# Kernel tuning notes

Measured on AMD Instinct MI355X. Metric: run time of the kernel, lower is better.

Reference implementation:

```python
import jax, jax.numpy as jnp
import numpy as np

NUM_USERS = 100000
NUM_BOOKS = 50000
HIDDEN = 128
USER_FEAT = 256
BOOK_FEAT = 256
E_PER_REL = 500000
NUM_LAYERS = 2


def setup_inputs() -> dict:
    key = jax.random.key(0)
    ks = jax.random.split(key, 10)
    user_x = jax.random.normal(ks[0], (NUM_USERS, USER_FEAT), dtype=jnp.float32)
    book_x = jax.random.normal(ks[1], (NUM_BOOKS, BOOK_FEAT), dtype=jnp.float32)
    user_W = jax.random.normal(ks[2], (HIDDEN, USER_FEAT), dtype=jnp.float32) * 0.05
    user_b = jax.random.normal(ks[3], (HIDDEN,), dtype=jnp.float32) * 0.05
    book_W = jax.random.normal(ks[4], (HIDDEN, BOOK_FEAT), dtype=jnp.float32) * 0.05
    book_b = jax.random.normal(ks[5], (HIDDEN,), dtype=jnp.float32) * 0.05
    # edge_index[0] = user indices, edge_index[1] = book indices
    rates_edge = jnp.stack([
        jax.random.randint(ks[6], (E_PER_REL,), 0, NUM_USERS),
        jax.random.randint(ks[7], (E_PER_REL,), 0, NUM_BOOKS)])
    implicit_edge = jnp.stack([
        jax.random.randint(ks[8], (E_PER_REL,), 0, NUM_USERS),
        jax.random.randint(ks[9], (E_PER_REL,), 0, NUM_BOOKS)])
    return {"user_x": user_x, "book_x": book_x, "user_W": user_W,
            "user_b": user_b, "book_W": book_W, "book_b": book_b,
            "rates_edge": rates_edge, "implicit_edge": implicit_edge}


def _lightgcn(user_x, book_x, user_W, user_b, book_W, book_b, rates_edge, implicit_edge):
    num_users = user_x.shape[0]
    num_nodes = num_users + book_x.shape[0]
    # input projections
    cu = user_x @ user_W.T + user_b  # [U, H]
    cb = book_x @ book_W.T + book_b  # [B, H]
    user_embeds = [cu]
    book_embeds = [cb]
    # build full directed edge list exactly as in the torch source
    all_edges = jnp.concatenate([rates_edge, implicit_edge], axis=1)  # [2, E]
    book_to_user = jnp.stack([all_edges[1] + num_users, all_edges[0]])
    full_edge = jnp.concatenate([all_edges, book_to_user], axis=1)  # [2, 2E]
    row, col = full_edge[0], full_edge[1]
    # symmetric degree normalization (edges fixed across layers)
    deg = jax.ops.segment_sum(jnp.ones(col.shape, dtype=cu.dtype), col,
                              num_segments=num_nodes)
    deg_inv_sqrt = jnp.where(deg > 0, jax.lax.rsqrt(jnp.maximum(deg, 1.0) * 0 + jnp.where(deg > 0, deg, 1.0)), 0.0)
    deg_inv_sqrt = jnp.where(deg > 0, jax.lax.rsqrt(jnp.where(deg > 0, deg, 1.0)), 0.0)
    norm = deg_inv_sqrt[row] * deg_inv_sqrt[col]  # [2E]
    for _ in range(NUM_LAYERS):
        x = jnp.concatenate([cu, cb], axis=0)  # [U+B, H]
        msg = x[row] * norm[:, None]           # gather + scale, [2E, H]
        out = jax.ops.segment_sum(msg, col, num_segments=num_nodes)  # scatter-add
        cu = out[:num_users]
        cb = out[num_users:]
        user_embeds.append(cu)
        book_embeds.append(cb)
    final_user = jnp.mean(jnp.stack(user_embeds), axis=0)
    final_book = jnp.mean(jnp.stack(book_embeds), axis=0)
    return final_user, final_book


def reference(user_x, book_x, user_W, user_b, book_W, book_b, rates_edge, implicit_edge):
    return _lightgcn(user_x, book_x, user_W, user_b, book_W, book_b,
                     rates_edge, implicit_edge)
```

## Files before the change

### kernel.cpp

```cpp
#include <hip/hip_runtime.h>

#define NUSERS 100000
#define NBOOKS 50000
#define HID 128
#define FEAT 256
#define EPR 500000
#define NEDGE (2 * EPR)

#define UBLK ((NUSERS + 127) / 128)
#define BBLK ((NBOOKS + 127) / 128)
#define GEMM_BLOCKS (UBLK + BBLK)
#define HIST_BLOCKS ((NEDGE + 1023) / 1024)

typedef __attribute__((ext_vector_type(8))) short bf16x8;
typedef __attribute__((ext_vector_type(4))) float f32x4;

__device__ __forceinline__ unsigned short f2bf(float f) {
  union { float f; unsigned u; } v; v.f = f;
  unsigned r = v.u + 0x7FFFu + ((v.u >> 16) & 1u);
  return (unsigned short)(r >> 16);
}
__device__ __forceinline__ float bf2f(unsigned short h) {
  union { unsigned u; float f; } v; v.u = ((unsigned)h) << 16;
  return v.f;
}

__global__ void cast_w(const float* __restrict__ w0, const float* __restrict__ w1,
                       unsigned short* __restrict__ o0, unsigned short* __restrict__ o1)
{
  int i = blockIdx.x * 256 + threadIdx.x;
  if (i < HID * FEAT) { o0[i] = f2bf(w0[i]); o1[i] = f2bf(w1[i]); }
}

__device__ __forceinline__ void decode_edge(const int* __restrict__ rates,
                                            const int* __restrict__ impl,
                                            int i, int& u, int& bk)
{
  if (i < EPR) { u = rates[i]; bk = rates[EPR + i]; }
  else { int j = i - EPR; u = impl[j]; bk = impl[EPR + j]; }
}

__global__ __launch_bounds__(256) void gemm_hist(
    const float* __restrict__ Xu, const float* __restrict__ Xb,
    const unsigned short* __restrict__ Wu, const unsigned short* __restrict__ Wb,
    const float* __restrict__ bu, const float* __restrict__ bb,
    unsigned short* __restrict__ cu0b, float* __restrict__ outb,
    float* __restrict__ outu,
    const int* __restrict__ rates, const int* __restrict__ impl,
    int* __restrict__ degu, int* __restrict__ cntb,
    unsigned int* __restrict__ relpos)
{
  __shared__ float Abuf[2][128 * 32];
  const int bid = blockIdx.x;
  const int tid = threadIdx.x;

  if (bid >= GEMM_BLOCKS) {
    const int hb = bid - GEMM_BLOCKS;
#pragma unroll
    for (int q = 0; q < 4; ++q) {
      int i = hb * 1024 + q * 256 + tid;
      if (i < NEDGE) {
        int u, bk;
        decode_edge(rates, impl, i, u, bk);
        relpos[i] = (unsigned int)atomicAdd(&cntb[bk], 1);
        atomicAdd(&degu[u], 1);
      }
    }
    return;
  }

  const bool isU = bid < UBLK;
  const float* __restrict__ X = isU ? Xu : Xb;
  const unsigned short* __restrict__ W = isU ? Wu : Wb;
  const float* __restrict__ bias = isU ? bu : bb;
  const int M  = isU ? NUSERS : NBOOKS;
  const int bm = (isU ? bid : bid - UBLK) * 128;

  const int lane = tid & 63;
  const int wv   = tid >> 6;
  const int l15  = lane & 15, l4 = lane >> 4;
  const int row0 = wv * 32;

  auto stage = [&](int bf, int ks) {
    const int k0 = ks * 32;
#pragma unroll
    for (int q = 0; q < 4; ++q) {
      int o = q * 256 + tid;
      int r = o >> 3;
      int s = (o & 7) ^ (r & 7);
      int gr = bm + r; if (gr > M - 1) gr = M - 1;
      const float* src = &X[(size_t)gr * FEAT + k0 + s * 4];
      float* dst = &Abuf[bf][(size_t)(q * 256 + wv * 64) * 4];
      __builtin_amdgcn_global_load_lds(src, dst, 16, 0, 0);
    }
  };

  f32x4 acc[2][8];
#pragma unroll
  for (int mi = 0; mi < 2; ++mi)
#pragma unroll
    for (int ni = 0; ni < 8; ++ni) acc[mi][ni] = (f32x4)0.f;

  stage(0, 0);

#pragma unroll
  for (int ks = 0; ks < 8; ++ks) {
    if (ks < 7) stage((ks + 1) & 1, ks + 1);
    __syncthreads();
    const float* Ab = Abuf[ks & 1];

    bf16x8 bfr[8];
#pragma unroll
    for (int ni = 0; ni < 8; ++ni) {
      int col = ni * 16 + l15;
      bfr[ni] = *reinterpret_cast<const bf16x8*>(&W[(size_t)col * FEAT + ks * 32 + l4 * 8]);
    }

    bf16x8 a[2];
#pragma unroll
    for (int mi = 0; mi < 2; ++mi) {
      int rt = row0 + mi * 16 + l15;
      int m7 = rt & 7;
      int s0 = l4 * 2;
      float4 x0 = *reinterpret_cast<const float4*>(&Ab[rt * 32 + ((s0)     ^ m7) * 4]);
      float4 x1 = *reinterpret_cast<const float4*>(&Ab[rt * 32 + ((s0 + 1) ^ m7) * 4]);
      bf16x8 av;
      av[0] = (short)f2bf(x0.x); av[1] = (short)f2bf(x0.y);
      av[2] = (short)f2bf(x0.z); av[3] = (short)f2bf(x0.w);
      av[4] = (short)f2bf(x1.x); av[5] = (short)f2bf(x1.y);
      av[6] = (short)f2bf(x1.z); av[7] = (short)f2bf(x1.w);
      a[mi] = av;
    }

#pragma unroll
    for (int ni = 0; ni < 8; ++ni) {
      acc[0][ni] = __builtin_amdgcn_mfma_f32_16x16x32_bf16(a[0], bfr[ni], acc[0][ni], 0, 0, 0);
      acc[1][ni] = __builtin_amdgcn_mfma_f32_16x16x32_bf16(a[1], bfr[ni], acc[1][ni], 0, 0, 0);
    }
    __syncthreads();
  }

#pragma unroll
  for (int ni = 0; ni < 8; ++ni) {
    int col = ni * 16 + l15;
    float bj = bias[col];
#pragma unroll
    for (int mi = 0; mi < 2; ++mi) {
#pragma unroll
      for (int j = 0; j < 4; ++j) {
        int rr = bm + row0 + mi * 16 + l4 * 4 + j;
        if (rr < M) {
          float vv = acc[mi][ni][j] + bj;
          if (isU) {
            cu0b[(size_t)rr * HID + col] = f2bf(vv);
            if (rr >= NBOOKS) outu[(size_t)rr * HID + col] = vv * (1.0f / 3.0f);
          } else {
            outb[(size_t)rr * HID + col] = vv * (1.0f / 3.0f);
          }
        }
      }
    }
  }
}

__global__ void dis_kernel(const int* __restrict__ degu, const int* __restrict__ cntb,
                           float* __restrict__ dis)
{
  int i = blockIdx.x * blockDim.x + threadIdx.x;
  if (i < NUSERS) {
    int d = degu[i] + (i < NBOOKS ? cntb[i] : 0);
    dis[i] = (d > 0) ? rsqrtf((float)d) : 0.f;
  }
}

__global__ void fill_scatter(const int* __restrict__ rates, const int* __restrict__ impl,
                             const int* __restrict__ offs,
                             const unsigned int* __restrict__ relpos,
                             int* __restrict__ brow)
{
  int i = blockIdx.x * blockDim.x + threadIdx.x;
  if (i >= NEDGE) return;
  int u, bk;
  decode_edge(rates, impl, i, u, bk);
  brow[offs[bk] + (int)relpos[i]] = u;
}

__global__ __launch_bounds__(1024) void scan_blocks(const int* __restrict__ counts,
                                                    int* __restrict__ offs,
                                                    int* __restrict__ bsum, int N)
{
  __shared__ int buf[1024];
  int t = threadIdx.x;
  int i = blockIdx.x * 1024 + t;
  int v = (i < N) ? counts[i] : 0;
  buf[t] = v;
  __syncthreads();
  for (int off = 1; off < 1024; off <<= 1) {
    int x = (t >= off) ? buf[t - off] : 0;
    __syncthreads();
    buf[t] += x;
    __syncthreads();
  }
  int incl = buf[t];
  if (i < N) offs[i] = incl - v;
  if (t == 1023) bsum[blockIdx.x] = incl;
}

__global__ void scan_totals(const int* __restrict__ bsum, int* __restrict__ bpre,
                            int* __restrict__ offs, int nb, int N)
{
  if (threadIdx.x == 0 && blockIdx.x == 0) {
    int run = 0;
    for (int b = 0; b < nb; ++b) { bpre[b] = run; run += bsum[b]; }
    offs[N] = run;
  }
}

__global__ void add_prefix(int* __restrict__ offs, const int* __restrict__ bpre, int N)
{
  int i = blockIdx.x * blockDim.x + threadIdx.x;
  if (i < N) offs[i] += bpre[i >> 10];
}

__global__ __launch_bounds__(256) void pull1(const unsigned short* __restrict__ srcb,
    const int* __restrict__ offs, const int* __restrict__ brow,
    const float* __restrict__ dis, unsigned short* __restrict__ dstb)
{
  int c = (blockIdx.x << 2) + (threadIdx.x >> 6);
  if (c >= NBOOKS) return;
  const int lane = threadIdx.x & 63;
  const int g = lane >> 4, l = lane & 15;
  const int s = offs[c], e = offs[c + 1];

  float acc[8];
#pragma unroll
  for (int j = 0; j < 8; ++j) acc[j] = 0.f;

  int i = s + g;
  for (; i + 4 < e; i += 8) {
    int rr0 = brow[i], rr1 = brow[i + 4];
    float w0 = dis[rr0], w1 = dis[rr1];
    bf16x8 v0 = *reinterpret_cast<const bf16x8*>(&srcb[(size_t)rr0 * HID + l * 8]);
    bf16x8 v1 = *reinterpret_cast<const bf16x8*>(&srcb[(size_t)rr1 * HID + l * 8]);
#pragma unroll
    for (int j = 0; j < 8; ++j) acc[j] += w0 * bf2f((unsigned short)v0[j]);
#pragma unroll
    for (int j = 0; j < 8; ++j) acc[j] += w1 * bf2f((unsigned short)v1[j]);
  }
  if (i < e) {
    int rr = brow[i];
    float w = dis[rr];
    bf16x8 v = *reinterpret_cast<const bf16x8*>(&srcb[(size_t)rr * HID + l * 8]);
#pragma unroll
    for (int j = 0; j < 8; ++j) acc[j] += w * bf2f((unsigned short)v[j]);
  }

#pragma unroll
  for (int j = 0; j < 8; ++j) {
    acc[j] += __shfl_xor(acc[j], 16, 64);
    acc[j] += __shfl_xor(acc[j], 32, 64);
  }
  if (g == 0) {
    float db = dis[c];
    bf16x8 o;
#pragma unroll
    for (int j = 0; j < 8; ++j) o[j] = (short)f2bf(db * acc[j]);
    *reinterpret_cast<bf16x8*>(&dstb[(size_t)c * HID + l * 8]) = o;
  }
}

__global__ __launch_bounds__(256) void pull2_final(const unsigned short* __restrict__ h1b,
    const int* __restrict__ offs, const int* __restrict__ brow,
    const float* __restrict__ dis, const unsigned short* __restrict__ cu0b,
    float* __restrict__ outu)
{
  int c = (blockIdx.x << 2) + (threadIdx.x >> 6);
  if (c >= NBOOKS) return;
  const int lane = threadIdx.x & 63;
  const int g = lane >> 4, l = lane & 15;
  const int s = offs[c], e = offs[c + 1];

  float acc[8];
#pragma unroll
  for (int j = 0; j < 8; ++j) acc[j] = 0.f;

  int i = s + g;
  for (; i + 4 < e; i += 8) {
    int rr0 = brow[i], rr1 = brow[i + 4];
    int rc0 = rr0 < NBOOKS ? rr0 : 0;
    int rc1 = rr1 < NBOOKS ? rr1 : 0;
    float w0 = rr0 < NBOOKS ? dis[rr0] : 0.f;
    float w1 = rr1 < NBOOKS ? dis[rr1] : 0.f;
    bf16x8 v0 = *reinterpret_cast<const bf16x8*>(&h1b[(size_t)rc0 * HID + l * 8]);
    bf16x8 v1 = *reinterpret_cast<const bf16x8*>(&h1b[(size_t)rc1 * HID + l * 8]);
#pragma unroll
    for (int j = 0; j < 8; ++j) acc[j] += w0 * bf2f((unsigned short)v0[j]);
#pragma unroll
    for (int j = 0; j < 8; ++j) acc[j] += w1 * bf2f((unsigned short)v1[j]);
  }
  if (i < e) {
    int rr = brow[i];
    int rc = rr < NBOOKS ? rr : 0;
    float w = rr < NBOOKS ? dis[rr] : 0.f;
    bf16x8 v = *reinterpret_cast<const bf16x8*>(&h1b[(size_t)rc * HID + l * 8]);
#pragma unroll
    for (int j = 0; j < 8; ++j) acc[j] += w * bf2f((unsigned short)v[j]);
  }

#pragma unroll
  for (int j = 0; j < 8; ++j) {
    acc[j] += __shfl_xor(acc[j], 16, 64);
    acc[j] += __shfl_xor(acc[j], 32, 64);
  }
  if (g == 0) {
    float db = dis[c];
    size_t idx = (size_t)c * HID + l * 8;
    bf16x8 c0 = *reinterpret_cast<const bf16x8*>(&cu0b[idx]);
    bf16x8 h1 = *reinterpret_cast<const bf16x8*>(&h1b[idx]);
    float r[8];
#pragma unroll
    for (int j = 0; j < 8; ++j)
      r[j] = (bf2f((unsigned short)c0[j]) + bf2f((unsigned short)h1[j]) + db * acc[j]) * (1.0f / 3.0f);
    *reinterpret_cast<float4*>(&outu[idx])     = make_float4(r[0], r[1], r[2], r[3]);
    *reinterpret_cast<float4*>(&outu[idx + 4]) = make_float4(r[4], r[5], r[6], r[7]);
  }
}

extern "C" void kernel_launch(void* const* d_in, const int* in_sizes, int n_in,
                              void* d_out, int out_size, void* d_ws, size_t ws_size,
                              hipStream_t stream)
{
  const float* user_x = (const float*)d_in[0];
  const float* book_x = (const float*)d_in[1];
  const float* user_W = (const float*)d_in[2];
  const float* user_b = (const float*)d_in[3];
  const float* book_W = (const float*)d_in[4];
  const float* book_b = (const float*)d_in[5];
  const int*   rates  = (const int*)d_in[6];
  const int*   impl   = (const int*)d_in[7];

  float* out      = (float*)d_out;
  float* out_user = out;
  float* out_book = out + (size_t)NUSERS * HID;

  char* p = (char*)d_ws;
  auto carve = [&](size_t bytes) -> void* {
    void* r = (void*)p;
    p += (bytes + 255) & ~(size_t)255;
    return r;
  };
  unsigned short* cu0b   = (unsigned short*)carve((size_t)NUSERS * HID * 2);
  unsigned short* h1b    = (unsigned short*)carve((size_t)NBOOKS * HID * 2);
  unsigned short* wub    = (unsigned short*)carve((size_t)HID * FEAT * 2);
  unsigned short* wbb    = (unsigned short*)carve((size_t)HID * FEAT * 2);
  int*          degu   = (int*)carve((size_t)NUSERS * 4);
  int*          cntb   = (int*)carve((size_t)NBOOKS * 4);
  float*        dis    = (float*)carve((size_t)NUSERS * 4);
  int*          offs   = (int*)carve((size_t)(NBOOKS + 2) * 4);
  int*          bsum   = (int*)carve(256 * 4);
  int*          bpre   = (int*)carve(256 * 4);
  unsigned int* relpos = (unsigned int*)carve((size_t)NEDGE * 4);
  int*          brow   = (int*)carve((size_t)NEDGE * 4);

  hipMemsetAsync(degu, 0, (size_t)NUSERS * 4, stream);
  hipMemsetAsync(cntb, 0, (size_t)NBOOKS * 4, stream);

  cast_w<<<(HID * FEAT + 255) / 256, 256, 0, stream>>>(user_W, book_W, wub, wbb);

  gemm_hist<<<GEMM_BLOCKS + HIST_BLOCKS, 256, 0, stream>>>(
      user_x, book_x, wub, wbb, user_b, book_b,
      cu0b, out_book, out_user, rates, impl, degu, cntb, relpos);

  dis_kernel<<<(NUSERS + 255) / 256, 256, 0, stream>>>(degu, cntb, dis);

  const int nb = (NBOOKS + 1023) / 1024;
  scan_blocks<<<nb, 1024, 0, stream>>>(cntb, offs, bsum, NBOOKS);
  scan_totals<<<1, 64, 0, stream>>>(bsum, bpre, offs, nb, NBOOKS);
  add_prefix<<<(NBOOKS + 255) / 256, 256, 0, stream>>>(offs, bpre, NBOOKS);
  fill_scatter<<<(NEDGE + 255) / 256, 256, 0, stream>>>(rates, impl, offs, relpos, brow);

  pull1<<<(NBOOKS + 3) / 4, 256, 0, stream>>>(cu0b, offs, brow, dis, h1b);
  pull2_final<<<(NBOOKS + 3) / 4, 256, 0, stream>>>(h1b, offs, brow, dis, cu0b, out_user);
}
```

Baseline: 258.9 us.

## Interleave histogram and GEMM blocks, stage bf16 A tile, fuse dis into fill

The combined GEMM/histogram kernel now interleaves histogram blocks with GEMM blocks so atomic-heavy edge counting runs concurrently with the projection instead of trailing it. The GEMM A tile is loaded through registers, converted to bf16 once, and stored in a swizzled 128x128 LDS buffer in two halves, replacing the double-buffered fp32 async-to-LDS pipeline and the per-iteration conversion. The degree inverse-sqrt kernel is merged into the edge fill-scatter launch to remove one launch. The change gives up async load overlap within the GEMM in exchange for fewer conversions and fewer barriers.

```diff
diff --git a/kernel.cpp b/kernel.cpp
--- a/kernel.cpp
+++ b/kernel.cpp
@@ -11,6 +11,8 @@
 #define BBLK ((NBOOKS + 127) / 128)
 #define GEMM_BLOCKS (UBLK + BBLK)
 #define HIST_BLOCKS ((NEDGE + 1023) / 1024)
+#define FILL_B ((NEDGE + 255) / 256)
+#define DIS_B ((NUSERS + 255) / 256)
 
 typedef __attribute__((ext_vector_type(8))) short bf16x8;
 typedef __attribute__((ext_vector_type(4))) float f32x4;
@@ -50,94 +52,100 @@
     int* __restrict__ degu, int* __restrict__ cntb,
     unsigned int* __restrict__ relpos)
 {
-  __shared__ float Abuf[2][128 * 32];
+  __shared__ unsigned short Asb[128 * 128];
   const int bid = blockIdx.x;
   const int tid = threadIdx.x;
 
-  if (bid >= GEMM_BLOCKS) {
-    const int hb = bid - GEMM_BLOCKS;
-#pragma unroll
-    for (int q = 0; q < 4; ++q) {
-      int i = hb * 1024 + q * 256 + tid;
-      if (i < NEDGE) {
-        int u, bk;
-        decode_edge(rates, impl, i, u, bk);
-        relpos[i] = (unsigned int)atomicAdd(&cntb[bk], 1);
-        atomicAdd(&degu[u], 1);
-      }
-    }
-    return;
-  }
-
-  const bool isU = bid < UBLK;
+  int gid;
+  if (bid < 2 * HIST_BLOCKS) {
+    if (bid & 1) {
+      const int hb = bid >> 1;
+#pragma unroll
+      for (int q = 0; q < 4; ++q) {
+        int i = hb * 1024 + q * 256 + tid;
+        if (i < NEDGE) {
+          int u, bk;
+          decode_edge(rates, impl, i, u, bk);
+          relpos[i] = (unsigned int)atomicAdd(&cntb[bk], 1);
+          atomicAdd(&degu[u], 1);
+        }
+      }
+      return;
+    }
+    gid = bid >> 1;
+  } else {
+    gid = bid - HIST_BLOCKS;
+  }
+
+  const bool isU = gid < UBLK;
   const float* __restrict__ X = isU ? Xu : Xb;
   const unsigned short* __restrict__ W = isU ? Wu : Wb;
   const float* __restrict__ bias = isU ? bu : bb;
   const int M  = isU ? NUSERS : NBOOKS;
-  const int bm = (isU ? bid : bid - UBLK) * 128;
+  const int bm = (isU ? gid : gid - UBLK) * 128;
 
   const int lane = tid & 63;
   const int wv   = tid >> 6;
   const int l15  = lane & 15, l4 = lane >> 4;
   const int row0 = wv * 32;
 
-  auto stage = [&](int bf, int ks) {
-    const int k0 = ks * 32;
-#pragma unroll
-    for (int q = 0; q < 4; ++q) {
-      int o = q * 256 + tid;
-      int r = o >> 3;
-      int s = (o & 7) ^ (r & 7);
-      int gr = bm + r; if (gr > M - 1) gr = M - 1;
-      const float* src = &X[(size_t)gr * FEAT + k0 + s * 4];
-      float* dst = &Abuf[bf][(size_t)(q * 256 + wv * 64) * 4];
-      __builtin_amdgcn_global_load_lds(src, dst, 16, 0, 0);
-    }
-  };
-
   f32x4 acc[2][8];
 #pragma unroll
   for (int mi = 0; mi < 2; ++mi)
 #pragma unroll
     for (int ni = 0; ni < 8; ++ni) acc[mi][ni] = (f32x4)0.f;
 
-  stage(0, 0);
-
-#pragma unroll
-  for (int ks = 0; ks < 8; ++ks) {
-    if (ks < 7) stage((ks + 1) & 1, ks + 1);
+#pragma unroll
+  for (int h = 0; h < 2; ++h) {
+    if (h) __syncthreads();
+
+#pragma unroll
+    for (int c8 = 0; c8 < 2; ++c8) {
+      float4 tmp[8];
+#pragma unroll
+      for (int k = 0; k < 8; ++k) {
+        int o = (c8 * 8 + k) * 256 + tid;
+        int row = o >> 5, c4 = o & 31;
+        int gr = bm + row; if (gr > M - 1) gr = M - 1;
+        tmp[k] = *reinterpret_cast<const float4*>(&X[(size_t)gr * FEAT + h * 128 + c4 * 4]);
+      }
+#pragma unroll
+      for (int k = 0; k < 8; ++k) {
+        int o = (c8 * 8 + k) * 256 + tid;
+        int row = o >> 5, c4 = o & 31;
+        int slot = (c4 >> 1) ^ (row & 15);
+        ushort4 w4;
+        w4.x = f2bf(tmp[k].x); w4.y = f2bf(tmp[k].y);
+        w4.z = f2bf(tmp[k].z); w4.w = f2bf(tmp[k].w);
+        *reinterpret_cast<ushort4*>(
+            reinterpret_cast<char*>(Asb) + row * 256 + slot * 16 + (c4 & 1) * 8) = w4;
+      }
+    }
     __syncthreads();
-    const float* Ab = Abuf[ks & 1];
-
-    bf16x8 bfr[8];
-#pragma unroll
-    for (int ni = 0; ni < 8; ++ni) {
-      int col = ni * 16 + l15;
-      bfr[ni] = *reinterpret_cast<const bf16x8*>(&W[(size_t)col * FEAT + ks * 32 + l4 * 8]);
-    }
-
-    bf16x8 a[2];
-#pragma unroll
-    for (int mi = 0; mi < 2; ++mi) {
-      int rt = row0 + mi * 16 + l15;
-      int m7 = rt & 7;
-      int s0 = l4 * 2;
-      float4 x0 = *reinterpret_cast<const float4*>(&Ab[rt * 32 + ((s0)     ^ m7) * 4]);
-      float4 x1 = *reinterpret_cast<const float4*>(&Ab[rt * 32 + ((s0 + 1) ^ m7) * 4]);
-      bf16x8 av;
-      av[0] = (short)f2bf(x0.x); av[1] = (short)f2bf(x0.y);
-      av[2] = (short)f2bf(x0.z); av[3] = (short)f2bf(x0.w);
-      av[4] = (short)f2bf(x1.x); av[5] = (short)f2bf(x1.y);
-      av[6] = (short)f2bf(x1.z); av[7] = (short)f2bf(x1.w);
-      a[mi] = av;
-    }
-
-#pragma unroll
-    for (int ni = 0; ni < 8; ++ni) {
-      acc[0][ni] = __builtin_amdgcn_mfma_f32_16x16x32_bf16(a[0], bfr[ni], acc[0][ni], 0, 0, 0);
-      acc[1][ni] = __builtin_amdgcn_mfma_f32_16x16x32_bf16(a[1], bfr[ni], acc[1][ni], 0, 0, 0);
-    }
-    __syncthreads();
+
+#pragma unroll
+    for (int ks = 0; ks < 4; ++ks) {
+      const int kg = h * 4 + ks;
+      bf16x8 bfr[8];
+#pragma unroll
+      for (int ni = 0; ni < 8; ++ni) {
+        int col = ni * 16 + l15;
+        bfr[ni] = *reinterpret_cast<const bf16x8*>(&W[(size_t)col * FEAT + kg * 32 + l4 * 8]);
+      }
+      bf16x8 a[2];
+#pragma unroll
+      for (int mi = 0; mi < 2; ++mi) {
+        int rt = row0 + mi * 16 + l15;
+        int slot = (ks * 4 + l4) ^ l15;
+        a[mi] = *reinterpret_cast<const bf16x8*>(
+            reinterpret_cast<const char*>(Asb) + rt * 256 + slot * 16);
+      }
+#pragma unroll
+      for (int ni = 0; ni < 8; ++ni) {
+        acc[0][ni] = __builtin_amdgcn_mfma_f32_16x16x32_bf16(a[0], bfr[ni], acc[0][ni], 0, 0, 0);
+        acc[1][ni] = __builtin_amdgcn_mfma_f32_16x16x32_bf16(a[1], bfr[ni], acc[1][ni], 0, 0, 0);
+      }
+    }
   }
 
 #pragma unroll
@@ -163,22 +171,23 @@
   }
 }
 
-__global__ void dis_kernel(const int* __restrict__ degu, const int* __restrict__ cntb,
-                           float* __restrict__ dis)
-{
-  int i = blockIdx.x * blockDim.x + threadIdx.x;
-  if (i < NUSERS) {
-    int d = degu[i] + (i < NBOOKS ? cntb[i] : 0);
-    dis[i] = (d > 0) ? rsqrtf((float)d) : 0.f;
-  }
-}
-
-__global__ void fill_scatter(const int* __restrict__ rates, const int* __restrict__ impl,
-                             const int* __restrict__ offs,
-                             const unsigned int* __restrict__ relpos,
-                             int* __restrict__ brow)
-{
-  int i = blockIdx.x * blockDim.x + threadIdx.x;
+__global__ void fill_dis(const int* __restrict__ rates, const int* __restrict__ impl,
+                         const int* __restrict__ offs,
+                         const unsigned int* __restrict__ relpos,
+                         int* __restrict__ brow,
+                         const int* __restrict__ degu, const int* __restrict__ cntb,
+                         float* __restrict__ dis)
+{
+  int b = blockIdx.x;
+  if (b >= FILL_B) {
+    int i = (b - FILL_B) * 256 + threadIdx.x;
+    if (i < NUSERS) {
+      int d = degu[i] + (i < NBOOKS ? cntb[i] : 0);
+      dis[i] = (d > 0) ? rsqrtf((float)d) : 0.f;
+    }
+    return;
+  }
+  int i = b * 256 + threadIdx.x;
   if (i >= NEDGE) return;
   int u, bk;
   decode_edge(rates, impl, i, u, bk);
@@ -371,13 +380,13 @@
       user_x, book_x, wub, wbb, user_b, book_b,
       cu0b, out_book, out_user, rates, impl, degu, cntb, relpos);
 
-  dis_kernel<<<(NUSERS + 255) / 256, 256, 0, stream>>>(degu, cntb, dis);
-
   const int nb = (NBOOKS + 1023) / 1024;
   scan_blocks<<<nb, 1024, 0, stream>>>(cntb, offs, bsum, NBOOKS);
   scan_totals<<<1, 64, 0, stream>>>(bsum, bpre, offs, nb, NBOOKS);
   add_prefix<<<(NBOOKS + 255) / 256, 256, 0, stream>>>(offs, bpre, NBOOKS);
-  fill_scatter<<<(NEDGE + 255) / 256, 256, 0, stream>>>(rates, impl, offs, relpos, brow);
+
+  fill_dis<<<FILL_B + DIS_B, 256, 0, stream>>>(rates, impl, offs, relpos, brow,
+                                               degu, cntb, dis);
 
   pull1<<<(NBOOKS + 3) / 4, 256, 0, stream>>>(cu0b, offs, brow, dis, h1b);
   pull2_final<<<(NBOOKS + 3) / 4, 256, 0, stream>>>(h1b, offs, brow, dis, cu0b, out_user);
```

New measurement: 271.4 us. +4.9%, slower.
